# Optimization experiments

Hardware: AMD Instinct MI355X
Metric: run time of the kernel (lower is better)

The kernel has to match this reference:

```python
import jax, jax.numpy as jnp
import numpy as np
import math

N = 32768
C = 128
K = 16
CHUNK = 2048
LN_EPS = float(C)  # original code calls torch.nn.LayerNorm(C, C): second positional arg is eps -> eps = 128.0 (faithful)


def knn_idx(coords):
    """Brute-force KNN on full coords [N,4] (matches knn_points(x_C, x_C, K=16)), chunked over queries."""
    def one_chunk(q):  # q: [CHUNK,4]
        d = jnp.sum((q[:, None, :] - coords[None, :, :]) ** 2, axis=-1)  # [CHUNK,N]
        return jax.lax.top_k(-d, K)[1]  # ascending distance (return_sorted=True)
    qs = coords.reshape(-1, CHUNK, coords.shape[-1])
    return jax.lax.map(one_chunk, qs).reshape(-1, K)  # [N,K]


def layer_norm(x, g, b):
    mu = jnp.mean(x, axis=-1, keepdims=True)
    var = jnp.mean((x - mu) ** 2, axis=-1, keepdims=True)
    return (x - mu) / jnp.sqrt(var + LN_EPS) * g + b


def self_attention(x_f, xyz_enc, new_feature, qw, qb, kw, kb, vw, vb):
    Q = x_f @ qw + qb                              # [N,C]
    nf = new_feature + xyz_enc                     # [N,K,C]
    Kt = nf @ kw + kb                              # [N,K,C]
    scores = jnp.einsum('nkd,nd->nk', Kt, Q) / math.sqrt(C)
    a = jax.nn.softmax(scores, axis=-1)            # [N,K]
    V = nf @ vw + vb                               # [N,K,C]
    return jnp.einsum('nk,nkd->nd', a, V)          # [N,C]


def setup_inputs() -> dict:
    key = jax.random.key(0)
    ks = jax.random.split(key, 22)
    xyz = jax.random.uniform(ks[0], (N, 3), dtype=jnp.float32) * 100.0
    coords = jnp.concatenate([jnp.zeros((N, 1), jnp.float32), xyz], axis=1)  # [N,4] batch col = 0
    feats = jax.random.normal(ks[1], (N, C), dtype=jnp.float32)
    s = 0.02
    def lin(k, din, dout):
        kw, kb = jax.random.split(k)
        return jax.random.normal(kw, (din, dout), jnp.float32) * s, jax.random.normal(kb, (dout,), jnp.float32) * s
    pos_w, pos_b = lin(ks[2], 3, C)
    pos1_w, pos1_b = lin(ks[3], 3, C)
    qw0, qb0 = lin(ks[4], C, C); kw0, kb0 = lin(ks[5], C, C); vw0, vb0 = lin(ks[6], C, C)
    qw1, qb1 = lin(ks[7], C, C); kw1, kb1 = lin(ks[8], C, C); vw1, vb1 = lin(ks[9], C, C)
    lin_w, lin_b = lin(ks[10], C, C)  # MinkowskiConvolution kernel_size=1 == pointwise linear
    return {
        'coords': coords, 'feats': feats,
        'pos_w': pos_w, 'pos_b': pos_b, 'pos1_w': pos1_w, 'pos1_b': pos1_b,
        'qw0': qw0, 'qb0': qb0, 'kw0': kw0, 'kb0': kb0, 'vw0': vw0, 'vb0': vb0,
        'qw1': qw1, 'qb1': qb1, 'kw1': kw1, 'kb1': kb1, 'vw1': vw1, 'vb1': vb1,
        'lin_w': lin_w, 'lin_b': lin_b,
        'g0': jnp.ones((C,), jnp.float32), 'be0': jnp.zeros((C,), jnp.float32),
        'g1': jnp.ones((C,), jnp.float32), 'be1': jnp.zeros((C,), jnp.float32),
    }


def reference(coords, feats, pos_w, pos_b, pos1_w, pos1_b,
              qw0, qb0, kw0, kb0, vw0, vb0,
              qw1, qb1, kw1, kb1, vw1, vb1,
              lin_w, lin_b, g0, be0, g1, be1):
    idx = knn_idx(coords)                           # [N,K]
    xyz = coords[:, 1:]                             # [N,3]
    new_xyz = xyz[:, None, :] - xyz[idx]            # [N,K,3] relative offsets
    # block 1
    xyz_enc = new_xyz @ pos_w + pos_b               # [N,K,C]
    nf = feats[idx]                                 # gather [N,K,C]
    o = self_attention(feats, xyz_enc, nf, qw0, qb0, kw0, kb0, vw0, vb0)
    # block 2: re-gather updated features with same idx
    nf1 = o[idx]
    xyz_enc1 = new_xyz @ pos1_w + pos1_b
    o = self_attention(o, xyz_enc1, nf1, qw1, qb1, kw1, kb1, vw1, vb1)
    # residual + LN, pointwise conv, residual + LN
    h = layer_norm(feats + o, g0, be0)
    h1 = h @ lin_w + lin_b
    return layer_norm(h + h1, g1, be1)
```

## Files before the change

### kernel.cpp

```cpp
#include <hip/hip_runtime.h>
#include <stdint.h>

#define NPT 32768

typedef unsigned int u32;
typedef unsigned short u16;
typedef unsigned long long u64;

typedef short v8s __attribute__((ext_vector_type(8)));
typedef float v4f __attribute__((ext_vector_type(4)));

__device__ __forceinline__ float b2f(u16 u) {
  union { u32 u; float f; } x; x.u = ((u32)u) << 16; return x.f;
}
__device__ __forceinline__ u16 f2b(float f) {
  union { float f; u32 u; } x; x.f = f;
  u32 u = x.u;
  return (u16)((u + 0x7fffu + ((u >> 16) & 1u)) >> 16);
}
__device__ __forceinline__ bool probe_f32(const void* coords) {
  return ((const u16*)coords)[1] == 0;
}
__device__ __forceinline__ float ldany(const void* p, long i, bool f32) {
  return f32 ? ((const float*)p)[i] : b2f(((const u16*)p)[i]);
}
__device__ __forceinline__ float wsum(float v) {
#pragma unroll
  for (int m = 1; m < 64; m <<= 1) v += __shfl_xor(v, m, 64);
  return v;
}

#define GC 16
#define GH 6.25f
#define GINV 0.16f
#define NCELL (GC * GC * GC)

__device__ __forceinline__ int cell1d(float v) {
  int c = (int)(v * GINV);
  return c > (GC - 1) ? (GC - 1) : (c < 0 ? 0 : c);
}

__global__ __launch_bounds__(256) void conv_coords_hist(const void* __restrict__ coords,
                                                        float* __restrict__ cx, float* __restrict__ cy,
                                                        float* __restrict__ cz, int* __restrict__ cellStart,
                                                        int* __restrict__ pcell) {
  const bool f32 = probe_f32(coords);
  int i = blockIdx.x * 256 + threadIdx.x;
  float x = ldany(coords, (long)i * 4 + 1, f32);
  float y = ldany(coords, (long)i * 4 + 2, f32);
  float z = ldany(coords, (long)i * 4 + 3, f32);
  cx[i] = x; cy[i] = y; cz[i] = z;
  int c = (cell1d(z) * GC + cell1d(y)) * GC + cell1d(x);
  pcell[i] = c;
  atomicAdd(&cellStart[c + 1], 1);
}

__global__ __launch_bounds__(256) void conv_featsS(const void* __restrict__ coords,
                                                   const void* __restrict__ feats,
                                                   const float4* __restrict__ sortedP,
                                                   u16* __restrict__ featsS) {
  const bool f32 = probe_f32(coords);
  long i = (long)blockIdx.x * 256 + threadIdx.x;
  int s = (int)(i >> 7), c = (int)(i & 127);
  long orig = (long)__float_as_int(sortedP[s].w);
  featsS[i] = f32 ? f2b(((const float*)feats)[orig * 128 + c]) : ((const u16*)feats)[orig * 128 + c];
}

__global__ __launch_bounds__(256) void grid_scan(int* __restrict__ cellStart, int* __restrict__ cellPtr) {
  __shared__ int part[256];
  const int t = threadIdx.x;
  int local[16]; int s = 0;
#pragma unroll
  for (int i = 0; i < 16; i++) { local[i] = cellStart[1 + t * 16 + i]; s += local[i]; }
  part[t] = s;
  __syncthreads();
  for (int off = 1; off < 256; off <<= 1) {
    int v = (t >= off) ? part[t - off] : 0;
    __syncthreads();
    part[t] += v;
    __syncthreads();
  }
  int run = (t == 0) ? 0 : part[t - 1];
#pragma unroll
  for (int i = 0; i < 16; i++) {
    int c = t * 16 + i;
    cellPtr[c] = run;
    run += local[i];
    cellStart[c + 1] = run;
  }
}

__global__ __launch_bounds__(256) void grid_scatter(const float* __restrict__ cx, const float* __restrict__ cy,
                                                    const float* __restrict__ cz, const int* __restrict__ pcell,
                                                    int* __restrict__ cellPtr, float4* __restrict__ sortedP,
                                                    int* __restrict__ rank) {
  int i = blockIdx.x * 256 + threadIdx.x;
  int c = pcell[i];
  int pos = atomicAdd(&cellPtr[c], 1);
  sortedP[pos] = make_float4(cx[i], cy[i], cz[i], __int_as_float(i));
  rank[i] = pos;
}

__global__ __launch_bounds__(256) void knn_grid(const float4* __restrict__ sortedP,
                                                const int* __restrict__ cellStart,
                                                const int* __restrict__ rank,
                                                u16* __restrict__ idxout) {
  const int lane = threadIdx.x & 63;
  const int gl = lane & 15;
  const int grp = lane >> 4;
  const int q = blockIdx.x * 16 + (threadIdx.x >> 4);
  const float4 p = sortedP[q];
  const float qx = p.x, qy = p.y, qz = p.z;
  const int qcx = cell1d(qx), qcy = cell1d(qy), qcz = cell1d(qz);

  u64 R = ~0ull;

  auto key_of = [&](int g) -> u64 {
    float4 sp = sortedP[g];
    float dx = __fsub_rn(qx, sp.x), dy = __fsub_rn(qy, sp.y), dzc = __fsub_rn(qz, sp.z);
    float d = __fadd_rn(__fadd_rn(__fmul_rn(dx, dx), __fmul_rn(dy, dy)), __fmul_rn(dzc, dzc));
    return ((u64)__float_as_uint(d) << 32) | (u32)__float_as_int(sp.w);
  };

  auto shfl64 = [&](u64 v, int s) -> u64 {
    int lo = __shfl((int)(u32)v, s, 16);
    int hi = __shfl((int)(u32)(v >> 32), s, 16);
    return ((u64)(u32)hi << 32) | (u32)lo;
  };
  auto sxg = [&](u64 v, int m) -> u64 {
    int lo = __shfl_xor((int)(u32)v, m, 64);
    int hi = __shfl_xor((int)(u32)(v >> 32), m, 64);
    return ((u64)(u32)hi << 32) | (u32)lo;
  };
  auto upg = [&](u64 v) -> u64 {
    int lo = __shfl_up((int)(u32)v, 1, 16);
    int hi = __shfl_up((int)(u32)(v >> 32), 1, 16);
    return ((u64)(u32)hi << 32) | (u32)lo;
  };

  auto insert_one = [&](u64 kk) {
    u64 prev = upg(R);
    if (gl == 0) prev = 0ull;
    R = (kk < R) ? ((kk >= prev) ? kk : prev) : R;
  };

  auto batch_merge = [&](u64 key) {
    u64 k15 = shfl64(R, 15);
    u64 mask = __ballot(key < k15);
    u32 mymask = (u32)((mask >> (grp * 16)) & 0xffffu);
    if (mymask == 0) return;
    int pcount = __popc(mymask);
    if (pcount <= 8) {
      u32 mm = mymask;
      while (mm) {
        int s = __ffs((int)mm) - 1;
        mm &= mm - 1;
        insert_one(shfl64(key, s));
      }
      return;
    }
#pragma unroll
    for (int k = 2; k <= 16; k <<= 1) {
#pragma unroll
      for (int j = k >> 1; j > 0; j >>= 1) {
        u64 o = sxg(key, j);
        bool up = ((gl & k) == 0);
        bool lower = ((gl & j) == 0);
        u64 mn = key < o ? key : o;
        u64 mx = key < o ? o : key;
        key = (lower == up) ? mn : mx;
      }
    }
    u64 s = sxg(key, 15);
    u64 mn = R < s ? R : s;
#pragma unroll
    for (int j = 8; j > 0; j >>= 1) {
      u64 o = sxg(mn, j);
      bool lower = ((gl & j) == 0);
      u64 lo = mn < o ? mn : o;
      u64 hi = mn < o ? o : mn;
      mn = lower ? lo : hi;
    }
    R = mn;
  };

  auto scan_range_grp = [&](int s0, int s1) {
    for (int base = s0; base < s1; base += 16) {
      int g = base + gl;
      u64 key = (g < s1) ? key_of(g) : ~0ull;
      batch_merge(key);
    }
  };

  {
    const int rord[9] = { 4, 1, 3, 5, 7, 0, 2, 6, 8 };
    int rs[9], rl[9];
#pragma unroll
    for (int s_ = 0; s_ < 9; s_++) {
      int row = rord[s_];
      int dz = row / 3 - 1, dy = row % 3 - 1;
      int z = qcz + dz, y = qcy + dy;
      if (z < 0 || z > GC - 1 || y < 0 || y > GC - 1) { rs[s_] = 0; rl[s_] = 0; }
      else {
        int rb = (z * GC + y) * GC;
        int xlo = qcx - 1 < 0 ? 0 : qcx - 1;
        int xhi = qcx + 1 > GC - 1 ? GC - 1 : qcx + 1;
        int s = cellStart[rb + xlo], e = cellStart[rb + xhi + 1];
        rs[s_] = s; rl[s_] = e - s;
      }
    }
    int cum[10]; cum[0] = 0;
#pragma unroll
    for (int i = 0; i < 9; i++) cum[i + 1] = cum[i] + rl[i];
    int total = cum[9];
    for (int base = 0; base < total; base += 16) {
      int pp = base + gl;
      u64 key = ~0ull;
      if (pp < total) {
        int g = 0;
#pragma unroll
        for (int i = 0; i < 9; i++) {
          if (pp >= cum[i] && pp < cum[i + 1]) g = rs[i] + (pp - cum[i]);
        }
        key = key_of(g);
      }
      batch_merge(key);
    }
  }

  {
    u64 k15 = shfl64(R, 15);
    float d15 = __uint_as_float((u32)(k15 >> 32));
    float b1 = GH * 1.0f;
    if (!(d15 < b1 * b1 * 0.998f)) {
      for (int r = 2; r < GC; ++r) {
        int zlo = qcz - r < 0 ? 0 : qcz - r, zhi = qcz + r > GC - 1 ? GC - 1 : qcz + r;
        for (int z = zlo; z <= zhi; ++z) {
          int adz = z - qcz; adz = adz < 0 ? -adz : adz;
          bool ez = (adz == r);
          int ylo = qcy - r < 0 ? 0 : qcy - r, yhi = qcy + r > GC - 1 ? GC - 1 : qcy + r;
          for (int y = ylo; y <= yhi; ++y) {
            int ady = y - qcy; ady = ady < 0 ? -ady : ady;
            bool ey = (ady == r);
            int rb = (z * GC + y) * GC;
            if (ez || ey) {
              int xlo = qcx - r < 0 ? 0 : qcx - r, xhi = qcx + r > GC - 1 ? GC - 1 : qcx + r;
              scan_range_grp(cellStart[rb + xlo], cellStart[rb + xhi + 1]);
            } else {
              int xm = qcx - r, xp = qcx + r;
              if (xm >= 0) scan_range_grp(cellStart[rb + xm], cellStart[rb + xm + 1]);
              if (xp <= GC - 1) scan_range_grp(cellStart[rb + xp], cellStart[rb + xp + 1]);
            }
          }
        }
        k15 = shfl64(R, 15);
        d15 = __uint_as_float((u32)(k15 >> 32));
        float bound = GH * (float)r;
        if (d15 < bound * bound * 0.998f) break;
      }
    }
  }

  idxout[(size_t)q * 16 + gl] = (u16)rank[(int)(u32)R];
}

__global__ __launch_bounds__(256) void prep_tables(
    const void* coords,
    const void* pw0, const void* pb0, const void* kw0, const void* kb0, const void* vw0, const void* vb0,
    const void* pw1, const void* pb1, const void* kw1, const void* kb1, const void* vw1, const void* vb1,
    float* __restrict__ tbl, int* __restrict__ cellStart) {
  const bool f32 = probe_f32(coords);
  const int tid = blockIdx.x * 256 + threadIdx.x;
  if (tid <= NCELL) cellStart[tid] = 0;
  const int lane = threadIdx.x & 63;
  const int o = blockIdx.x * 4 + (threadIdx.x >> 6);
  const int l = o >> 10;
  const int rem = o & 1023;
  const void* PW = l ? pw1 : pw0;
  const void* PB = l ? pb1 : pb0;
  const void* KW = l ? kw1 : kw0;
  const void* KB = l ? kb1 : kb0;
  const void* VW = l ? vw1 : vw0;
  const void* VB = l ? vb1 : vb0;
  float acc, extra = 0.f;
  if (rem < 768) {
    bool isV = rem >= 384;
    int r2 = isV ? rem - 384 : rem;
    int i = r2 >> 7, c = r2 & 127;
    const void* W = isV ? VW : KW;
    acc = ldany(PW, i * 128 + lane, f32) * ldany(W, (long)lane * 128 + c, f32)
        + ldany(PW, i * 128 + lane + 64, f32) * ldany(W, (long)(lane + 64) * 128 + c, f32);
  } else {
    bool isV = rem >= 896;
    int c = rem & 127;
    const void* W = isV ? VW : KW;
    const void* B = isV ? VB : KB;
    acc = ldany(PB, lane, f32) * ldany(W, (long)lane * 128 + c, f32)
        + ldany(PB, lane + 64, f32) * ldany(W, (long)(lane + 64) * 128 + c, f32);
    extra = ldany(B, c, f32);
  }
  acc = wsum(acc) + extra;
  if (lane == 0) tbl[l * 1024 + rem] = acc;
}

__global__ __launch_bounds__(256) void prep_bfrag_all(const void* __restrict__ coords,
                                                      const void* __restrict__ qw0, const void* __restrict__ kw0,
                                                      const void* __restrict__ vw0, const void* __restrict__ qw1,
                                                      const void* __restrict__ kw1, const void* __restrict__ vw1,
                                                      const void* __restrict__ linw, u16* __restrict__ Bf0,
                                                      u16* __restrict__ Bf1, u16* __restrict__ BfL) {
  const bool f32 = probe_f32(coords);
  int tid = blockIdx.x * 256 + threadIdx.x;
  const void *w0, *w1, *w2; u16* out; int t;
  if (tid < 49152) { t = tid; w0 = qw0; w1 = kw0; w2 = vw0; out = Bf0; }
  else if (tid < 98304) { t = tid - 49152; w0 = qw1; w1 = kw1; w2 = vw1; out = Bf1; }
  else { t = tid - 98304; w0 = linw; w1 = linw; w2 = linw; out = BfL; }
  int j = t & 7, lane = (t >> 3) & 63, kq = (t >> 9) & 3, tile = t >> 11;
  int k = kq * 32 + ((lane >> 4) << 3) + j;
  int col = tile * 16 + (lane & 15);
  const void* w = (col < 128) ? w0 : ((col < 256) ? w1 : w2);
  long off = (long)k * 128 + (col & 127);
  out[t] = f32 ? f2b(((const float*)w)[off]) : ((const u16*)w)[off];
}

__global__ __launch_bounds__(256) void gemm_kernel(const void* __restrict__ coords,
                                                   const u16* __restrict__ A, const u16* __restrict__ Bf,
                                                   const void* __restrict__ bias, u16* __restrict__ Qb,
                                                   u16* __restrict__ KVb, float* __restrict__ outF,
                                                   const float* __restrict__ tblp, float* __restrict__ pOut,
                                                   int mode, int ntiles) {
  const bool f32 = probe_f32(coords);
  const int lane = threadIdx.x & 63;
  const int wave = threadIdx.x >> 6;
  const int r0 = blockIdx.x * 64 + wave * 16;
  const int quad = lane >> 4, lr = lane & 15;
  v8s a[4];
#pragma unroll
  for (int kq = 0; kq < 4; kq++) {
    union { uint4 u; v8s s; } c;
    c.u = *(const uint4*)(A + (size_t)(r0 + lr) * 128 + kq * 32 + quad * 8);
    a[kq] = c.s;
  }
  float pd0[4] = { 0.f, 0.f, 0.f, 0.f };
  float pd1[4] = { 0.f, 0.f, 0.f, 0.f };
  float pd2[4] = { 0.f, 0.f, 0.f, 0.f };
  float pd3[4] = { 0.f, 0.f, 0.f, 0.f };
  for (int tile = 0; tile < ntiles; ++tile) {
    v4f acc = { 0.f, 0.f, 0.f, 0.f };
#pragma unroll
    for (int kq = 0; kq < 4; kq++) {
      union { uint4 u; v8s s; } c;
      c.u = *(const uint4*)(Bf + ((size_t)(tile * 4 + kq) * 64 + lane) * 8);
      acc = __builtin_amdgcn_mfma_f32_16x16x32_bf16(a[kq], c.s, acc, 0, 0, 0);
    }
    int col = tile * 16 + lr;
    if (mode == 0) {
      if (col < 128) {
        float bb = ldany(bias, col, f32);
        float t0 = tblp[col], t1 = tblp[128 + col], t2 = tblp[256 + col], t3 = tblp[768 + col];
#pragma unroll
        for (int r = 0; r < 4; r++) {
          float qv = acc[r] + bb;
          Qb[(size_t)(r0 + quad * 4 + r) * 128 + col] = f2b(qv);
          pd0[r] += t0 * qv;
          pd1[r] += t1 * qv;
          pd2[r] += t2 * qv;
          pd3[r] += t3 * qv;
        }
      } else {
#pragma unroll
        for (int r = 0; r < 4; r++) KVb[(size_t)(r0 + quad * 4 + r) * 256 + (col - 128)] = f2b(acc[r]);
      }
    } else {
      float bb = ldany(bias, col, f32);
#pragma unroll
      for (int r = 0; r < 4; r++) outF[(size_t)(r0 + quad * 4 + r) * 128 + col] = acc[r] + bb;
    }
  }
  if (mode == 0) {
#pragma unroll
    for (int m = 1; m < 16; m <<= 1) {
#pragma unroll
      for (int r = 0; r < 4; r++) {
        pd0[r] += __shfl_xor(pd0[r], m, 64);
        pd1[r] += __shfl_xor(pd1[r], m, 64);
        pd2[r] += __shfl_xor(pd2[r], m, 64);
        pd3[r] += __shfl_xor(pd3[r], m, 64);
      }
    }
    if (lr < 4) {
#pragma unroll
      for (int r = 0; r < 4; r++) {
        float v = (lr == 0) ? pd0[r] : ((lr == 1) ? pd1[r] : ((lr == 2) ? pd2[r] : pd3[r]));
        pOut[(size_t)(r0 + quad * 4 + r) * 4 + lr] = v;
      }
    }
  }
}

__global__ __launch_bounds__(256) void attn_kernel(const void* __restrict__ coordsRaw,
                                                   const float4* __restrict__ sortedP,
                                                   const u16* __restrict__ idx,
                                                   const u16* __restrict__ Qb, const u16* __restrict__ KVb,
                                                   const float* __restrict__ tbl, const float* __restrict__ p4,
                                                   const void* __restrict__ feats,
                                                   const void* __restrict__ g, const void* __restrict__ be,
                                                   u16* __restrict__ outB, int mode) {
  const int lane = threadIdx.x & 63;
  const int swz = (blockIdx.x & 7) * (gridDim.x >> 3) + (blockIdx.x >> 3);
  const int n = swz * 4 + (threadIdx.x >> 6);
  const int c0 = 2 * lane;
  const int k = lane & 15;
  const int quad = lane >> 4;
  const int base = lane & 48;

  const int j = idx[(size_t)n * 16 + k];
  u32 vr[16];
#pragma unroll
  for (int k2 = 0; k2 < 16; k2++) {
    int jk = __shfl(j, base + k2, 64);
    vr[k2] = *(const u32*)(KVb + (size_t)jk * 256 + 128 + c0);
  }
  uint4 kf[4];
#pragma unroll
  for (int kq = 0; kq < 4; kq++) {
    kf[kq] = *(const uint4*)(KVb + (size_t)j * 256 + kq * 32 + quad * 8);
  }
  const float4 P = sortedP[n];
  const float4 Pj = sortedP[j];
  const float nx = P.x - Pj.x, ny = P.y - Pj.y, nz = P.z - Pj.z;
  const float4 pv = *(const float4*)(p4 + (size_t)n * 4);

  v4f sacc = { 0.f, 0.f, 0.f, 0.f };
#pragma unroll
  for (int kq = 0; kq < 4; kq++) {
    union { uint4 u; v8s s; } ka, qa;
    ka.u = kf[kq];
    qa.u = *(const uint4*)(Qb + (size_t)n * 128 + kq * 32 + quad * 8);
    sacc = __builtin_amdgcn_mfma_f32_16x16x32_bf16(ka.s, qa.s, sacc, 0, 0, 0);
  }
  const int srcl = ((k >> 2) << 4) | k;
  float t0 = __shfl(sacc[0], srcl, 64);
  float t1 = __shfl(sacc[1], srcl, 64);
  float t2 = __shfl(sacc[2], srcl, 64);
  float t3 = __shfl(sacc[3], srcl, 64);
  float s = (k & 2) ? ((k & 1) ? t3 : t2) : ((k & 1) ? t1 : t0);
  float sc = (s + nx * pv.x + ny * pv.y + nz * pv.z + pv.w) * 0.08838834764831845f;

  float mx = sc;
#pragma unroll
  for (int m = 1; m < 16; m <<= 1) mx = fmaxf(mx, __shfl_xor(mx, m, 64));
  float e = expf(sc - mx);
  float ssum = e;
#pragma unroll
  for (int m = 1; m < 16; m <<= 1) ssum += __shfl_xor(ssum, m, 64);
  const float a = e / ssum;

  float wx = a * nx, wy = a * ny, wz = a * nz;
#pragma unroll
  for (int m = 1; m < 16; m <<= 1) {
    wx += __shfl_xor(wx, m, 64);
    wy += __shfl_xor(wy, m, 64);
    wz += __shfl_xor(wz, m, 64);
  }

  float a0 = 0.f, a1 = 0.f;
#pragma unroll
  for (int k2 = 0; k2 < 16; k2++) {
    float ak = __shfl(a, base + k2, 64);
    u32 u = vr[k2];
    a0 += ak * b2f((u16)(u & 0xffffu));
    a1 += ak * b2f((u16)(u >> 16));
  }
  float o0 = a0 + wx * tbl[384 + c0] + wy * tbl[512 + c0] + wz * tbl[640 + c0] + tbl[896 + c0];
  float o1 = a1 + wx * tbl[384 + c0 + 1] + wy * tbl[512 + c0 + 1] + wz * tbl[640 + c0 + 1] + tbl[896 + c0 + 1];
  if (mode == 1) {
    const bool f32 = probe_f32(coordsRaw);
    long orig = (long)__float_as_int(P.w);
    float x0 = ldany(feats, orig * 128 + c0, f32) + o0;
    float x1 = ldany(feats, orig * 128 + c0 + 1, f32) + o1;
    float mu = wsum(x0 + x1) * (1.f / 128.f);
    float d0 = x0 - mu, d1 = x1 - mu;
    float var = wsum(d0 * d0 + d1 * d1) * (1.f / 128.f);
    float rinv = 1.0f / sqrtf(var + 128.0f);
    o0 = d0 * rinv * ldany(g, c0, f32) + ldany(be, c0, f32);
    o1 = d1 * rinv * ldany(g, c0 + 1, f32) + ldany(be, c0 + 1, f32);
  }
  ((u32*)outB)[(size_t)n * 64 + lane] = (u32)f2b(o0) | ((u32)f2b(o1) << 16);
}

__global__ __launch_bounds__(256) void ln_final(const void* __restrict__ coords,
                                                const float4* __restrict__ sortedP,
                                                const u16* __restrict__ hB, const float* __restrict__ h1F,
                                                const void* __restrict__ g, const void* __restrict__ be,
                                                void* __restrict__ outAny) {
  const bool f32 = probe_f32(coords);
  const int lane = threadIdx.x & 63;
  const int n = blockIdx.x * 4 + (threadIdx.x >> 6);
  const int c0 = 2 * lane;
  u32 u = *(const u32*)(hB + (size_t)n * 128 + c0);
  float2 h1 = *(const float2*)(h1F + (size_t)n * 128 + c0);
  float x0 = b2f((u16)(u & 0xffffu)) + h1.x;
  float x1 = b2f((u16)(u >> 16)) + h1.y;
  float mu = wsum(x0 + x1) * (1.f / 128.f);
  float d0 = x0 - mu, d1 = x1 - mu;
  float var = wsum(d0 * d0 + d1 * d1) * (1.f / 128.f);
  float rinv = 1.0f / sqrtf(var + 128.0f);
  float y0 = d0 * rinv * ldany(g, c0, f32) + ldany(be, c0, f32);
  float y1 = d1 * rinv * ldany(g, c0 + 1, f32) + ldany(be, c0 + 1, f32);
  size_t orig = (size_t)__float_as_int(sortedP[n].w);
  if (f32) {
    *(float2*)((float*)outAny + orig * 128 + c0) = make_float2(y0, y1);
  } else {
    ((u32*)outAny)[orig * 64 + lane] = (u32)f2b(y0) | ((u32)f2b(y1) << 16);
  }
}

extern "C" void kernel_launch(void* const* d_in, const int* in_sizes, int n_in,
                              void* d_out, int out_size, void* d_ws, size_t ws_size,
                              hipStream_t stream) {
  (void)in_sizes; (void)n_in; (void)out_size; (void)ws_size;
  const void* coords = d_in[0];
  const void* feats = d_in[1];
  const void* pos_w = d_in[2];
  const void* pos_b = d_in[3];
  const void* pos1_w = d_in[4];
  const void* pos1_b = d_in[5];
  const void* qw0 = d_in[6];
  const void* qb0 = d_in[7];
  const void* kw0 = d_in[8];
  const void* kb0 = d_in[9];
  const void* vw0 = d_in[10];
  const void* vb0 = d_in[11];
  const void* qw1 = d_in[12];
  const void* qb1 = d_in[13];
  const void* kw1 = d_in[14];
  const void* kb1 = d_in[15];
  const void* vw1 = d_in[16];
  const void* vb1 = d_in[17];
  const void* lin_w = d_in[18];
  const void* lin_b = d_in[19];
  const void* g0 = d_in[20];
  const void* be0 = d_in[21];
  const void* g1 = d_in[22];
  const void* be1 = d_in[23];

  char* w = (char*)d_ws;
  u16* idxp = (u16*)(w + 0);
  float4* sortedP = (float4*)(w + 1048576);
  int* rank = (int*)(w + 1572864);
  float* cx = (float*)(w + 1703936);
  float* cy = (float*)(w + 1835008);
  float* cz = (float*)(w + 1966080);
  float* tbl = (float*)(w + 2097152);
  u16* Bf0 = (u16*)(w + 2105344);
  u16* Bf1 = (u16*)(w + 2203648);
  u16* BfL = (u16*)(w + 2301952);
  u16* featsS = (u16*)(w + 2334720);
  u16* oS = (u16*)(w + 10723328);
  u16* Qb = (u16*)(w + 19111936);
  u16* KVb = (u16*)(w + 27500544);
  int* cellStart = (int*)(w + 19111936);
  int* cellPtr = (int*)(w + 19132416);
  int* pcell = (int*)(w + 19148800);
  float* h1F = (float*)(w + 19111936);
  float* p4 = (float*)(w + 1572864);

  hipLaunchKernelGGL(prep_tables, dim3(512), dim3(256), 0, stream, coords,
                     pos_w, pos_b, kw0, kb0, vw0, vb0, pos1_w, pos1_b, kw1, kb1, vw1, vb1, tbl, cellStart);
  hipLaunchKernelGGL(conv_coords_hist, dim3(128), dim3(256), 0, stream, coords, cx, cy, cz, cellStart, pcell);
  hipLaunchKernelGGL(prep_bfrag_all, dim3(448), dim3(256), 0, stream, coords,
                     qw0, kw0, vw0, qw1, kw1, vw1, lin_w, Bf0, Bf1, BfL);

  hipLaunchKernelGGL(grid_scan, dim3(1), dim3(256), 0, stream, cellStart, cellPtr);
  hipLaunchKernelGGL(grid_scatter, dim3(128), dim3(256), 0, stream, cx, cy, cz, pcell, cellPtr, sortedP, rank);
  hipLaunchKernelGGL(conv_featsS, dim3(16384), dim3(256), 0, stream, coords, feats, sortedP, featsS);
  hipLaunchKernelGGL(knn_grid, dim3(2048), dim3(256), 0, stream, sortedP, cellStart, rank, idxp);

  hipLaunchKernelGGL(gemm_kernel, dim3(512), dim3(256), 0, stream, coords, featsS, Bf0, qb0, Qb, KVb,
                     (float*)nullptr, tbl, p4, 0, 24);
  hipLaunchKernelGGL(attn_kernel, dim3(8192), dim3(256), 0, stream, coords, sortedP, idxp, Qb, KVb, tbl, p4,
                     (const void*)nullptr, (const void*)nullptr, (const void*)nullptr, oS, 0);
  hipLaunchKernelGGL(gemm_kernel, dim3(512), dim3(256), 0, stream, coords, oS, Bf1, qb1, Qb, KVb,
                     (float*)nullptr, tbl + 1024, p4, 0, 24);
  hipLaunchKernelGGL(attn_kernel, dim3(8192), dim3(256), 0, stream, coords, sortedP, idxp, Qb, KVb, tbl + 1024, p4,
                     feats, g0, be0, oS, 1);
  hipLaunchKernelGGL(gemm_kernel, dim3(512), dim3(256), 0, stream, coords, oS, BfL, lin_b,
                     (u16*)nullptr, (u16*)nullptr, h1F, (const float*)nullptr, (float*)nullptr, 1, 8);
  hipLaunchKernelGGL(ln_final, dim3(8192), dim3(256), 0, stream, coords, sortedP, oS, h1F, g1, be1, d_out);
}
```

Baseline: 322.7 us.

## Fuse KNN and first GEMM into one launch, gather feats directly in GEMM

Removes the conv_featsS kernel: the first GEMM now gathers rows of the original feats through the sorted permutation and converts them to bf16 on the fly. KNN and the first GEMM are merged into one grid, with the first 2048 blocks doing KNN and the rest the GEMM, so the two independent stages can overlap. The KNN scan loops are also software-pipelined, loading the next batch's key before merging the current one. Workspace offsets are rearranged so cellStart no longer aliases the Qb region written by the fused GEMM, at the cost of more register pressure and a less uniform workload in the combined kernel.

```diff
diff --git a/kernel.cpp b/kernel.cpp
--- a/kernel.cpp
+++ b/kernel.cpp
@@ -28,6 +28,21 @@
 #pragma unroll
   for (int m = 1; m < 64; m <<= 1) v += __shfl_xor(v, m, 64);
   return v;
+}
+__device__ __forceinline__ v8s ldA8(const void* feats, long row, int off, bool f32) {
+  union { uint4 u; v8s s; } c;
+  if (f32) {
+    const float* f = (const float*)feats + row * 128 + off;
+    float4 x = *(const float4*)f;
+    float4 y = *(const float4*)(f + 4);
+    c.u.x = (u32)f2b(x.x) | ((u32)f2b(x.y) << 16);
+    c.u.y = (u32)f2b(x.z) | ((u32)f2b(x.w) << 16);
+    c.u.z = (u32)f2b(y.x) | ((u32)f2b(y.y) << 16);
+    c.u.w = (u32)f2b(y.z) | ((u32)f2b(y.w) << 16);
+  } else {
+    c.u = *(const uint4*)((const u16*)feats + row * 128 + off);
+  }
+  return c.s;
 }
 
 #define GC 16
@@ -55,17 +70,6 @@
   atomicAdd(&cellStart[c + 1], 1);
 }
 
-__global__ __launch_bounds__(256) void conv_featsS(const void* __restrict__ coords,
-                                                   const void* __restrict__ feats,
-                                                   const float4* __restrict__ sortedP,
-                                                   u16* __restrict__ featsS) {
-  const bool f32 = probe_f32(coords);
-  long i = (long)blockIdx.x * 256 + threadIdx.x;
-  int s = (int)(i >> 7), c = (int)(i & 127);
-  long orig = (long)__float_as_int(sortedP[s].w);
-  featsS[i] = f32 ? f2b(((const float*)feats)[orig * 128 + c]) : ((const u16*)feats)[orig * 128 + c];
-}
-
 __global__ __launch_bounds__(256) void grid_scan(int* __restrict__ cellStart, int* __restrict__ cellPtr) {
   __shared__ int part[256];
   const int t = threadIdx.x;
@@ -101,14 +105,15 @@
   rank[i] = pos;
 }
 
-__global__ __launch_bounds__(256) void knn_grid(const float4* __restrict__ sortedP,
-                                                const int* __restrict__ cellStart,
-                                                const int* __restrict__ rank,
-                                                u16* __restrict__ idxout) {
-  const int lane = threadIdx.x & 63;
+__device__ __forceinline__ void knn_body(int blk, int tid,
+                                         const float4* __restrict__ sortedP,
+                                         const int* __restrict__ cellStart,
+                                         const int* __restrict__ rank,
+                                         u16* __restrict__ idxout) {
+  const int lane = tid & 63;
   const int gl = lane & 15;
   const int grp = lane >> 4;
-  const int q = blockIdx.x * 16 + (threadIdx.x >> 4);
+  const int q = blk * 16 + (tid >> 4);
   const float4 p = sortedP[q];
   const float qx = p.x, qy = p.y, qz = p.z;
   const int qcx = cell1d(qx), qcy = cell1d(qy), qcz = cell1d(qz);
@@ -185,10 +190,14 @@
   };
 
   auto scan_range_grp = [&](int s0, int s1) {
+    if (s0 >= s1) return;
+    int g0 = s0 + gl;
+    u64 key = (g0 < s1) ? key_of(g0) : ~0ull;
     for (int base = s0; base < s1; base += 16) {
-      int g = base + gl;
-      u64 key = (g < s1) ? key_of(g) : ~0ull;
+      int gn = base + 16 + gl;
+      u64 nkey = (base + 16 < s1) ? ((gn < s1) ? key_of(gn) : ~0ull) : ~0ull;
       batch_merge(key);
+      key = nkey;
     }
   };
 
@@ -213,18 +222,20 @@
 #pragma unroll
     for (int i = 0; i < 9; i++) cum[i + 1] = cum[i] + rl[i];
     int total = cum[9];
+    auto keyat = [&](int pp) -> u64 {
+      if (pp >= total) return ~0ull;
+      int g = 0;
+#pragma unroll
+      for (int i = 0; i < 9; i++) {
+        if (pp >= cum[i] && pp < cum[i + 1]) g = rs[i] + (pp - cum[i]);
+      }
+      return key_of(g);
+    };
+    u64 key = keyat(gl);
     for (int base = 0; base < total; base += 16) {
-      int pp = base + gl;
-      u64 key = ~0ull;
-      if (pp < total) {
-        int g = 0;
-#pragma unroll
-        for (int i = 0; i < 9; i++) {
-          if (pp >= cum[i] && pp < cum[i + 1]) g = rs[i] + (pp - cum[i]);
-        }
-        key = key_of(g);
-      }
+      u64 nkey = (base + 16 < total) ? keyat(base + 16 + gl) : ~0ull;
       batch_merge(key);
+      key = nkey;
     }
   }
 
@@ -262,6 +273,116 @@
   }
 
   idxout[(size_t)q * 16 + gl] = (u16)rank[(int)(u32)R];
+}
+
+__device__ __forceinline__ void gemm_body(int blk, int tid, const void* coords,
+                                          const u16* __restrict__ A, const void* __restrict__ featsAny,
+                                          const float4* __restrict__ sortedPtr,
+                                          const u16* __restrict__ Bf, const void* __restrict__ bias,
+                                          u16* __restrict__ Qb, u16* __restrict__ KVb,
+                                          float* __restrict__ outF,
+                                          const float* __restrict__ tblp, float* __restrict__ pOut,
+                                          int mode, int ntiles) {
+  const bool f32 = probe_f32(coords);
+  const int lane = tid & 63;
+  const int wave = tid >> 6;
+  const int r0 = blk * 64 + wave * 16;
+  const int quad = lane >> 4, lr = lane & 15;
+  v8s a[4];
+  if (sortedPtr) {
+    long arow = (long)__float_as_int(sortedPtr[r0 + lr].w);
+#pragma unroll
+    for (int kq = 0; kq < 4; kq++) a[kq] = ldA8(featsAny, arow, kq * 32 + quad * 8, f32);
+  } else {
+#pragma unroll
+    for (int kq = 0; kq < 4; kq++) {
+      union { uint4 u; v8s s; } c;
+      c.u = *(const uint4*)(A + (size_t)(r0 + lr) * 128 + kq * 32 + quad * 8);
+      a[kq] = c.s;
+    }
+  }
+  float pd0[4] = { 0.f, 0.f, 0.f, 0.f };
+  float pd1[4] = { 0.f, 0.f, 0.f, 0.f };
+  float pd2[4] = { 0.f, 0.f, 0.f, 0.f };
+  float pd3[4] = { 0.f, 0.f, 0.f, 0.f };
+  for (int tile = 0; tile < ntiles; ++tile) {
+    v4f acc = { 0.f, 0.f, 0.f, 0.f };
+#pragma unroll
+    for (int kq = 0; kq < 4; kq++) {
+      union { uint4 u; v8s s; } c;
+      c.u = *(const uint4*)(Bf + ((size_t)(tile * 4 + kq) * 64 + lane) * 8);
+      acc = __builtin_amdgcn_mfma_f32_16x16x32_bf16(a[kq], c.s, acc, 0, 0, 0);
+    }
+    int col = tile * 16 + lr;
+    if (mode == 0) {
+      if (col < 128) {
+        float bb = ldany(bias, col, f32);
+        float t0 = tblp[col], t1 = tblp[128 + col], t2 = tblp[256 + col], t3 = tblp[768 + col];
+#pragma unroll
+        for (int r = 0; r < 4; r++) {
+          float qv = acc[r] + bb;
+          Qb[(size_t)(r0 + quad * 4 + r) * 128 + col] = f2b(qv);
+          pd0[r] += t0 * qv;
+          pd1[r] += t1 * qv;
+          pd2[r] += t2 * qv;
+          pd3[r] += t3 * qv;
+        }
+      } else {
+#pragma unroll
+        for (int r = 0; r < 4; r++) KVb[(size_t)(r0 + quad * 4 + r) * 256 + (col - 128)] = f2b(acc[r]);
+      }
+    } else {
+      float bb = ldany(bias, col, f32);
+#pragma unroll
+      for (int r = 0; r < 4; r++) outF[(size_t)(r0 + quad * 4 + r) * 128 + col] = acc[r] + bb;
+    }
+  }
+  if (mode == 0) {
+#pragma unroll
+    for (int m = 1; m < 16; m <<= 1) {
+#pragma unroll
+      for (int r = 0; r < 4; r++) {
+        pd0[r] += __shfl_xor(pd0[r], m, 64);
+        pd1[r] += __shfl_xor(pd1[r], m, 64);
+        pd2[r] += __shfl_xor(pd2[r], m, 64);
+        pd3[r] += __shfl_xor(pd3[r], m, 64);
+      }
+    }
+    if (lr < 4) {
+#pragma unroll
+      for (int r = 0; r < 4; r++) {
+        float v = (lr == 0) ? pd0[r] : ((lr == 1) ? pd1[r] : ((lr == 2) ? pd2[r] : pd3[r]));
+        pOut[(size_t)(r0 + quad * 4 + r) * 4 + lr] = v;
+      }
+    }
+  }
+}
+
+__global__ __launch_bounds__(256) void knn_gemm0(const float4* __restrict__ sortedP,
+                                                 const int* __restrict__ cellStart,
+                                                 const int* __restrict__ rank,
+                                                 u16* __restrict__ idxout,
+                                                 const void* __restrict__ coords,
+                                                 const void* __restrict__ feats,
+                                                 const u16* __restrict__ Bf, const void* __restrict__ bias,
+                                                 u16* __restrict__ Qb, u16* __restrict__ KVb,
+                                                 const float* __restrict__ tblp, float* __restrict__ pOut) {
+  if (blockIdx.x < 2048) {
+    knn_body(blockIdx.x, threadIdx.x, sortedP, cellStart, rank, idxout);
+  } else {
+    gemm_body(blockIdx.x - 2048, threadIdx.x, coords, (const u16*)nullptr, feats, sortedP,
+              Bf, bias, Qb, KVb, (float*)nullptr, tblp, pOut, 0, 24);
+  }
+}
+
+__global__ __launch_bounds__(256) void gemm_kernel(const void* __restrict__ coords,
+                                                   const u16* __restrict__ A, const u16* __restrict__ Bf,
+                                                   const void* __restrict__ bias, u16* __restrict__ Qb,
+                                                   u16* __restrict__ KVb, float* __restrict__ outF,
+                                                   const float* __restrict__ tblp, float* __restrict__ pOut,
+                                                   int mode, int ntiles) {
+  gemm_body(blockIdx.x, threadIdx.x, coords, A, (const void*)nullptr, (const float4*)nullptr,
+            Bf, bias, Qb, KVb, outF, tblp, pOut, mode, ntiles);
 }
 
 __global__ __launch_bounds__(256) void prep_tables(
@@ -323,81 +444,6 @@
   out[t] = f32 ? f2b(((const float*)w)[off]) : ((const u16*)w)[off];
 }
 
-__global__ __launch_bounds__(256) void gemm_kernel(const void* __restrict__ coords,
-                                                   const u16* __restrict__ A, const u16* __restrict__ Bf,
-                                                   const void* __restrict__ bias, u16* __restrict__ Qb,
-                                                   u16* __restrict__ KVb, float* __restrict__ outF,
-                                                   const float* __restrict__ tblp, float* __restrict__ pOut,
-                                                   int mode, int ntiles) {
-  const bool f32 = probe_f32(coords);
-  const int lane = threadIdx.x & 63;
-  const int wave = threadIdx.x >> 6;
-  const int r0 = blockIdx.x * 64 + wave * 16;
-  const int quad = lane >> 4, lr = lane & 15;
-  v8s a[4];
-#pragma unroll
-  for (int kq = 0; kq < 4; kq++) {
-    union { uint4 u; v8s s; } c;
-    c.u = *(const uint4*)(A + (size_t)(r0 + lr) * 128 + kq * 32 + quad * 8);
-    a[kq] = c.s;
-  }
-  float pd0[4] = { 0.f, 0.f, 0.f, 0.f };
-  float pd1[4] = { 0.f, 0.f, 0.f, 0.f };
-  float pd2[4] = { 0.f, 0.f, 0.f, 0.f };
-  float pd3[4] = { 0.f, 0.f, 0.f, 0.f };
-  for (int tile = 0; tile < ntiles; ++tile) {
-    v4f acc = { 0.f, 0.f, 0.f, 0.f };
-#pragma unroll
-    for (int kq = 0; kq < 4; kq++) {
-      union { uint4 u; v8s s; } c;
-      c.u = *(const uint4*)(Bf + ((size_t)(tile * 4 + kq) * 64 + lane) * 8);
-      acc = __builtin_amdgcn_mfma_f32_16x16x32_bf16(a[kq], c.s, acc, 0, 0, 0);
-    }
-    int col = tile * 16 + lr;
-    if (mode == 0) {
-      if (col < 128) {
-        float bb = ldany(bias, col, f32);
-        float t0 = tblp[col], t1 = tblp[128 + col], t2 = tblp[256 + col], t3 = tblp[768 + col];
-#pragma unroll
-        for (int r = 0; r < 4; r++) {
-          float qv = acc[r] + bb;
-          Qb[(size_t)(r0 + quad * 4 + r) * 128 + col] = f2b(qv);
-          pd0[r] += t0 * qv;
-          pd1[r] += t1 * qv;
-          pd2[r] += t2 * qv;
-          pd3[r] += t3 * qv;
-        }
-      } else {
-#pragma unroll
-        for (int r = 0; r < 4; r++) KVb[(size_t)(r0 + quad * 4 + r) * 256 + (col - 128)] = f2b(acc[r]);
-      }
-    } else {
-      float bb = ldany(bias, col, f32);
-#pragma unroll
-      for (int r = 0; r < 4; r++) outF[(size_t)(r0 + quad * 4 + r) * 128 + col] = acc[r] + bb;
-    }
-  }
-  if (mode == 0) {
-#pragma unroll
-    for (int m = 1; m < 16; m <<= 1) {
-#pragma unroll
-      for (int r = 0; r < 4; r++) {
-        pd0[r] += __shfl_xor(pd0[r], m, 64);
-        pd1[r] += __shfl_xor(pd1[r], m, 64);
-        pd2[r] += __shfl_xor(pd2[r], m, 64);
-        pd3[r] += __shfl_xor(pd3[r], m, 64);
-      }
-    }
-    if (lr < 4) {
-#pragma unroll
-      for (int r = 0; r < 4; r++) {
-        float v = (lr == 0) ? pd0[r] : ((lr == 1) ? pd1[r] : ((lr == 2) ? pd2[r] : pd3[r]));
-        pOut[(size_t)(r0 + quad * 4 + r) * 4 + lr] = v;
-      }
-    }
-  }
-}
-
 __global__ __launch_bounds__(256) void attn_kernel(const void* __restrict__ coordsRaw,
                                                    const float4* __restrict__ sortedP,
                                                    const u16* __restrict__ idx,
@@ -556,15 +602,14 @@
   u16* Bf0 = (u16*)(w + 2105344);
   u16* Bf1 = (u16*)(w + 2203648);
   u16* BfL = (u16*)(w + 2301952);
-  u16* featsS = (u16*)(w + 2334720);
+  float* p4 = (float*)(w + 2334720);
+  int* cellStart = (int*)(w + 2859008);
+  int* cellPtr = (int*)(w + 2875456);
+  int* pcell = (int*)(w + 2891840);
   u16* oS = (u16*)(w + 10723328);
   u16* Qb = (u16*)(w + 19111936);
   u16* KVb = (u16*)(w + 27500544);
-  int* cellStart = (int*)(w + 19111936);
-  int* cellPtr = (int*)(w + 19132416);
-  int* pcell = (int*)(w + 19148800);
   float* h1F = (float*)(w + 19111936);
-  float* p4 = (float*)(w + 1572864);
 
   hipLaunchKernelGGL(prep_tables, dim3(512), dim3(256), 0, stream, coords,
                      pos_w, pos_b, kw0, kb0, vw0, vb0, pos1_w, pos1_b, kw1, kb1, vw1, vb1, tbl, cellStart);
@@ -574,11 +619,10 @@
 
   hipLaunchKernelGGL(grid_scan, dim3(1), dim3(256), 0, stream, cellStart, cellPtr);
   hipLaunchKernelGGL(grid_scatter, dim3(128), dim3(256), 0, stream, cx, cy, cz, pcell, cellPtr, sortedP, rank);
-  hipLaunchKernelGGL(conv_featsS, dim3(16384), dim3(256), 0, stream, coords, feats, sortedP, featsS);
-  hipLaunchKernelGGL(knn_grid, dim3(2048), dim3(256), 0, stream, sortedP, cellStart, rank, idxp);
-
-  hipLaunchKernelGGL(gemm_kernel, dim3(512), dim3(256), 0, stream, coords, featsS, Bf0, qb0, Qb, KVb,
-                     (float*)nullptr, tbl, p4, 0, 24);
+
+  hipLaunchKernelGGL(knn_gemm0, dim3(2560), dim3(256), 0, stream, sortedP, cellStart, rank, idxp,
+                     coords, feats, Bf0, qb0, Qb, KVb, tbl, p4);
+
   hipLaunchKernelGGL(attn_kernel, dim3(8192), dim3(256), 0, stream, coords, sortedP, idxp, Qb, KVb, tbl, p4,
                      (const void*)nullptr, (const void*)nullptr, (const void*)nullptr, oS, 0);
   hipLaunchKernelGGL(gemm_kernel, dim3(512), dim3(256), 0, stream, coords, oS, Bf1, qb1, Qb, KVb,
```

New measurement: 300.8 us. 1.07x faster.
